# Kernel tuning notes

Measured on AMD Instinct MI355X. Metric: run time of the kernel, lower is better.

## Reference

```python
import jax, jax.numpy as jnp
import numpy as np

N, T = 32, 1500
ENC_DIM, DEC_DIM = 1024, 1024
ATT_DIM, ATT_HEAD = 512, 4
HA = ATT_DIM * ATT_HEAD


def setup_inputs() -> dict:
    key = jax.random.key(0)
    ks = jax.random.split(key, 12)
    enc_pad = jax.random.normal(ks[0], (N, T, ENC_DIM), dtype=jnp.float32)
    enc_len = jax.random.randint(ks[1], (N,), T // 2, T + 1)
    enc_len = enc_len.at[0].set(T)  # ensure max == T (original code assumes mask width == T)
    dec_prev = jax.random.normal(ks[2], (N, DEC_DIM), dtype=jnp.float32)
    ali_prev = jnp.zeros((N, T), dtype=jnp.float32)  # unused by forward
    s = 0.02
    W_enc = jax.random.normal(ks[3], (ENC_DIM, HA), dtype=jnp.float32) * s
    b_enc = jnp.zeros((HA,), dtype=jnp.float32)
    W_key = jax.random.normal(ks[4], (ENC_DIM, HA), dtype=jnp.float32) * s
    W_dec = jax.random.normal(ks[5], (DEC_DIM, HA), dtype=jnp.float32) * s
    W_ctx = jax.random.normal(ks[6], (HA, ENC_DIM), dtype=jnp.float32) * s
    b_ctx = jnp.zeros((ENC_DIM,), dtype=jnp.float32)
    # grouped Conv1d(HA -> H, kernel=1, groups=H, bias=False): weight [H, A]
    w_conv = jax.random.normal(ks[7], (ATT_HEAD, ATT_DIM), dtype=jnp.float32) * s
    return dict(enc_pad=enc_pad, enc_len=enc_len, dec_prev=dec_prev, ali_prev=ali_prev,
                W_enc=W_enc, b_enc=b_enc, W_key=W_key, W_dec=W_dec,
                W_ctx=W_ctx, b_ctx=b_ctx, w_conv=w_conv)


def reference(enc_pad, enc_len, dec_prev, ali_prev,
              W_enc, b_enc, W_key, W_dec, W_ctx, b_ctx, w_conv):
    n, t, _ = enc_pad.shape
    H, A = ATT_HEAD, ATT_DIM
    # enc_part: N x H x T x A
    enc_part = (enc_pad @ W_enc + b_enc).reshape(n, t, H, A).transpose(0, 2, 1, 3)
    # key_part: N x H x A x T
    key_part = (enc_pad @ W_key).reshape(n, t, H, A).transpose(0, 2, 3, 1)
    # dec_part: N x H x A
    dec_part = (dec_prev @ W_dec).reshape(n, H, A)
    # additive score: tanh(key + dec), grouped 1x1 conv scorer -> N x H x T
    sum_part = jnp.tanh(key_part + dec_part[:, :, :, None])
    e = jnp.einsum('nhat,ha->nht', sum_part, w_conv)
    # padding mask: True where t >= enc_len
    pad_mask = jnp.arange(t)[None, :] >= enc_len[:, None]  # N x T
    e = jnp.where(pad_mask[:, None, :], -jnp.inf, e)
    ali = jax.nn.softmax(e, axis=-1)  # N x H x T
    # weighted sum over time, then context projection
    ctx = jnp.einsum('nht,nhta->nha', ali, enc_part).reshape(n, H * A)
    ctx = ctx @ W_ctx + b_ctx  # N x D_enc
    return ali, ctx
```

## Files before the change

kernel.cpp:

```cpp
#include <hip/hip_runtime.h>
#include <hip/hip_bf16.h>


#define N_B   32
#define T_S   1500
#define ENC_D 1024
#define HA_D  2048
#define A_D   512
#define H_N   4
#define MROWS 48000

typedef short s8v  __attribute__((ext_vector_type(8)));
typedef float f32x4 __attribute__((ext_vector_type(4)));

__device__ __forceinline__ unsigned short f2bf(float f) {
    unsigned u = __float_as_uint(f);
    unsigned r = (u + 0x7FFFu + ((u >> 16) & 1u)) >> 16;
    return (unsigned short)r;
}
__device__ __forceinline__ float bf2f(unsigned short b) {
    return __uint_as_float(((unsigned)b) << 16);
}
__device__ __forceinline__ float fast_tanh(float x) {
    float e2 = __expf(2.0f * x);
    return 1.0f - __fdividef(2.0f, e2 + 1.0f);
}
__device__ __forceinline__ void gload_lds16(const void* g, void* l) {
    __builtin_amdgcn_global_load_lds(
        (const unsigned int __attribute__((address_space(1)))*)g,
        (unsigned int __attribute__((address_space(3)))*)l, 16, 0, 0);
}

__device__ __forceinline__ void skinny_body(
    int bid, const float* __restrict__ X, const float* __restrict__ W,
    const float* __restrict__ bias, float* __restrict__ Y,
    int Ncols, int ct_mask, int ct_shift, int xA, int xB, float* xT ) {
    const int tid = threadIdx.x;
    const int ct = bid & ct_mask, ks = bid >> ct_shift;
    const int c0 = ct << 8, k0 = ks << 6;
    const int hsel = c0 >> 9;
    {
        const int n = tid >> 3, kk0 = (tid & 7) << 3;
        const float* xr = X + (size_t)n * xA + hsel * xB + k0 + kk0;
        float4 v0 = *(const float4*)xr;
        float4 v1 = *(const float4*)(xr + 4);
        xT[(kk0 + 0) * 36 + n] = v0.x;
        xT[(kk0 + 1) * 36 + n] = v0.y;
        xT[(kk0 + 2) * 36 + n] = v0.z;
        xT[(kk0 + 3) * 36 + n] = v0.w;
        xT[(kk0 + 4) * 36 + n] = v1.x;
        xT[(kk0 + 5) * 36 + n] = v1.y;
        xT[(kk0 + 6) * 36 + n] = v1.z;
        xT[(kk0 + 7) * 36 + n] = v1.w;
    }
    __syncthreads();
    const int w = tid >> 6, lane = tid & 63;
    f32x4 acc[8];
    if (bias != nullptr && ks == 0) {
        f32x4 bv = *(const f32x4*)&bias[c0 + (lane << 2)];
#pragma unroll
        for (int j = 0; j < 8; ++j) acc[j] = bv;
    } else {
#pragma unroll
        for (int j = 0; j < 8; ++j) { f32x4 z = {0.f, 0.f, 0.f, 0.f}; acc[j] = z; }
    }
    const float* Wp = W + (size_t)k0 * Ncols + c0 + (lane << 2);
#pragma unroll 4
    for (int kk = 0; kk < 64; ++kk) {
        f32x4 wf = *(const f32x4*)(Wp + (size_t)kk * Ncols);
        f32x4 xlo = *(const f32x4*)&xT[kk * 36 + w * 8];
        f32x4 xhi = *(const f32x4*)&xT[kk * 36 + w * 8 + 4];
#pragma unroll
        for (int j = 0; j < 4; ++j) {
            acc[j]     += xlo[j] * wf;
            acc[4 + j] += xhi[j] * wf;
        }
    }
#pragma unroll
    for (int j = 0; j < 8; ++j) {
        float* yp = Y + (size_t)(w * 8 + j) * Ncols + c0 + (lane << 2);
#pragma unroll
        for (int i = 0; i < 4; ++i) atomicAdd(yp + i, acc[j][i]);
    }
}

__global__ __launch_bounds__(256) void skinny_k(
    const float* __restrict__ X, const float* __restrict__ W,
    const float* __restrict__ bias, float* __restrict__ Y,
    int Ncols, int ct_mask, int ct_shift, int xA, int xB) {
    __shared__ float xT[64 * 36];
    skinny_body(blockIdx.x, X, W, bias, Y, Ncols, ct_mask, ct_shift, xA, xB, xT);
}

__global__ __launch_bounds__(256) void prep_k(
    const float* __restrict__ enc_pad, const float* __restrict__ Wk,
    const float* __restrict__ dec_prev, const float* __restrict__ W_dec,
    unsigned short* __restrict__ Xb, unsigned short* __restrict__ Wt,
    float* __restrict__ dp) {
    __shared__ float shmem[64 * 65];
    const int b = blockIdx.x;
    const int tid = threadIdx.x;
    if (b < 128) {
        skinny_body(b, dec_prev, W_dec, nullptr, dp, HA_D, 7, 3, 1024, 0, shmem);
    } else if (b < 640) {
        float (*ld)[65] = (float(*)[65])shmem;
        const int bb = b - 128;
        const int tx = tid & 63, ty = tid >> 6;
        const int c0 = (bb & 31) * 64, d0 = (bb >> 5) * 64;
#pragma unroll
        for (int j = 0; j < 16; ++j)
            ld[ty + 4 * j][tx] = Wk[(size_t)(d0 + ty + 4 * j) * HA_D + c0 + tx];
        __syncthreads();
#pragma unroll
        for (int j = 0; j < 16; ++j)
            Wt[(size_t)(c0 + ty + 4 * j) * ENC_D + d0 + tx] = f2bf(ld[tx][ty + 4 * j]);
    } else {
        const float4* in = (const float4*)enc_pad;
        ushort4* out = (ushort4*)Xb;
        for (int i = (b - 640) * 256 + tid; i < 12288000; i += 3000 * 256) {
            float4 v = in[i];
            ushort4 o;
            o.x = f2bf(v.x); o.y = f2bf(v.y); o.z = f2bf(v.z); o.w = f2bf(v.w);
            out[i] = o;
        }
    }
}

__global__ __launch_bounds__(512) void fused_score_k(
    const unsigned short* __restrict__ Xb, const unsigned short* __restrict__ Wt,
    const float* __restrict__ dec, const float* __restrict__ wconv,
    const int* __restrict__ enc_len, float* __restrict__ e_out) {
    __shared__ unsigned short As[128 * 64];
    __shared__ unsigned short Bs[256 * 64];
    __shared__ float e_s[128];

    const int tid = threadIdx.x;
    const int lane = tid & 63, wid = tid >> 6;
    const int wr = wid >> 2, wc = wid & 3;
    const int l15 = lane & 15, lhi = lane >> 4;

    int orig = blockIdx.x;
    int wgid = (orig & 7) * 375 + (orig >> 3);
    const int mtile = wgid >> 3, nt = wgid & 7;
    const int r0 = mtile * 128;
    const int bcol0 = nt * 256;
    const int h = nt >> 1;

    {
        int n0 = (int)((unsigned)r0 / 1500u);
        int t0 = r0 - n0 * 1500;
        if (t0 + 127 < 1500 && t0 >= enc_len[n0]) return;
    }

    if (tid < 128) e_s[tid] = 0.f;

    const unsigned short* aSrc[2]; int aDst[2];
#pragma unroll
    for (int ld = 0; ld < 2; ++ld) {
        int li = ld * 512 + tid, rowL = li >> 3, c16 = li & 7;
        aSrc[ld] = Xb + (size_t)(r0 + rowL) * ENC_D + ((c16 ^ (rowL & 7)) << 3);
        aDst[ld] = li * 8;
    }
    const unsigned short* bSrc[4]; int bDst[4];
#pragma unroll
    for (int ld = 0; ld < 4; ++ld) {
        int li = ld * 512 + tid, colL = li >> 3, c16 = li & 7;
        bSrc[ld] = Wt + (size_t)(bcol0 + colL) * ENC_D + ((c16 ^ (colL & 7)) << 3);
        bDst[ld] = li * 8;
    }

    const int cA0 = (lhi * 8) ^ ((l15 & 7) << 3);
    const int cA1 = (32 + lhi * 8) ^ ((l15 & 7) << 3);
    const int arow = wr * 64 + l15;
    const int bcol = wc * 64 + l15;

    f32x4 acc[4][4];
#pragma unroll
    for (int m = 0; m < 4; ++m)
#pragma unroll
        for (int n2 = 0; n2 < 4; ++n2) {
            f32x4 z = {0.f, 0.f, 0.f, 0.f};
            acc[m][n2] = z;
        }

    for (int ks = 0; ks < 16; ++ks) {
        const int kb = ks << 6;
#pragma unroll
        for (int ld = 0; ld < 2; ++ld) gload_lds16(aSrc[ld] + kb, As + aDst[ld]);
#pragma unroll
        for (int ld = 0; ld < 4; ++ld) gload_lds16(bSrc[ld] + kb, Bs + bDst[ld]);
        __syncthreads();
#pragma unroll
        for (int kk = 0; kk < 2; ++kk) {
            const int cc = kk ? cA1 : cA0;
            s8v af[4], bv[4];
#pragma unroll
            for (int m = 0; m < 4; ++m)
                af[m] = *(const s8v*)&As[(arow + m * 16) * 64 + cc];
#pragma unroll
            for (int n2 = 0; n2 < 4; ++n2)
                bv[n2] = *(const s8v*)&Bs[(bcol + n2 * 16) * 64 + cc];
#pragma unroll
            for (int m = 0; m < 4; ++m)
#pragma unroll
                for (int n2 = 0; n2 < 4; ++n2)
                    acc[m][n2] = __builtin_amdgcn_mfma_f32_16x16x32_bf16(af[m], bv[n2], acc[m][n2], 0, 0, 0);
        }
        __syncthreads();
    }

    float wv[4];
#pragma unroll
    for (int n2 = 0; n2 < 4; ++n2)
        wv[n2] = wconv[bcol0 + wc * 64 + n2 * 16 + l15];
#pragma unroll
    for (int m = 0; m < 4; ++m) {
#pragma unroll
        for (int rg = 0; rg < 4; ++rg) {
            int row_l = wr * 64 + m * 16 + lhi * 4 + rg;
            int grow = r0 + row_l;
            int nn = (int)((unsigned)grow / 1500u);
            const float* dsl = dec + (size_t)nn * HA_D + bcol0 + wc * 64 + l15;
            float s = 0.f;
#pragma unroll
            for (int n2 = 0; n2 < 4; ++n2) {
                float v = acc[m][n2][rg] + dsl[n2 * 16];
                s += wv[n2] * fast_tanh(v);
            }
            s += __shfl_xor(s, 1); s += __shfl_xor(s, 2);
            s += __shfl_xor(s, 4); s += __shfl_xor(s, 8);
            if (l15 == 0) atomicAdd(&e_s[row_l], s);
        }
    }
    __syncthreads();
    if (tid < 128) {
        int grow = r0 + tid;
        int nn = grow / 1500, tt = grow - nn * 1500;
        atomicAdd(&e_out[(size_t)(nn * H_N + h) * T_S + tt], e_s[tid]);
    }
}

__global__ void softmax_k(const float* __restrict__ e, const int* __restrict__ enc_len,
                          float* __restrict__ ali, float* __restrict__ ctx_zero) {
    const int tid = threadIdx.x, lane = tid & 63, wid = tid >> 6;
    ctx_zero[blockIdx.x * 256 + tid] = 0.f;
    const int n = blockIdx.x >> 2;
    const int len = enc_len[n];
    const float* row = e + (size_t)blockIdx.x * T_S;
    float* orow = ali + (size_t)blockIdx.x * T_S;
    __shared__ float red[4];
    float p[6];
    float mx = -__builtin_inff();
#pragma unroll
    for (int i = 0; i < 6; ++i) {
        int t = tid + i * 256;
        float v = -__builtin_inff();
        if (t < T_S && t < len) v = row[t];
        p[i] = v;
        mx = fmaxf(mx, v);
    }
#pragma unroll
    for (int o = 32; o; o >>= 1) mx = fmaxf(mx, __shfl_xor(mx, o));
    if (lane == 0) red[wid] = mx;
    __syncthreads();
    mx = fmaxf(fmaxf(red[0], red[1]), fmaxf(red[2], red[3]));
    __syncthreads();
    float sum = 0.f;
#pragma unroll
    for (int i = 0; i < 6; ++i) {
        float qv = (p[i] == -__builtin_inff()) ? 0.f : __expf(p[i] - mx);
        p[i] = qv;
        sum += qv;
    }
#pragma unroll
    for (int o = 32; o; o >>= 1) sum += __shfl_xor(sum, o);
    if (lane == 0) red[wid] = sum;
    __syncthreads();
    sum = red[0] + red[1] + red[2] + red[3];
    float inv = 1.0f / sum;
#pragma unroll
    for (int i = 0; i < 6; ++i) {
        int t = tid + i * 256;
        if (t < T_S) orow[t] = p[i] * inv;
    }
}

__global__ __launch_bounds__(256) void wenc_k(const unsigned short* __restrict__ Xb,
                                              const float* __restrict__ ali,
                                              const int* __restrict__ enc_len,
                                              float* __restrict__ wenc) {
    const int tid = threadIdx.x;
    const int n = blockIdx.x & 31, tq = blockIdx.x >> 5;
    const int t0 = tq * 94;
    const int tcnt = (t0 + 94 <= T_S) ? 94 : (T_S - t0);
    if (t0 >= enc_len[n]) return;
    __shared__ float alis[4][94];
    for (int i = tid; i < 376; i += 256) {
        int hh = i / 94, tt = i - hh * 94;
        if (tt < tcnt) alis[hh][tt] = ali[(size_t)(n * H_N + hh) * T_S + t0 + tt];
    }
    __syncthreads();
    const int d0 = tid * 4;
    float a[4][4] = {};
    const unsigned short* xp = Xb + (size_t)(n * T_S + t0) * ENC_D + d0;
#pragma unroll 4
    for (int t = 0; t < tcnt; ++t) {
        ushort4 xv = *(const ushort4*)&xp[(size_t)t * ENC_D];
        float x0 = bf2f(xv.x), x1 = bf2f(xv.y), x2 = bf2f(xv.z), x3 = bf2f(xv.w);
#pragma unroll
        for (int hh = 0; hh < 4; ++hh) {
            float al = alis[hh][t];
            a[hh][0] = fmaf(al, x0, a[hh][0]);
            a[hh][1] = fmaf(al, x1, a[hh][1]);
            a[hh][2] = fmaf(al, x2, a[hh][2]);
            a[hh][3] = fmaf(al, x3, a[hh][3]);
        }
    }
#pragma unroll
    for (int hh = 0; hh < 4; ++hh)
#pragma unroll
        for (int j = 0; j < 4; ++j)
            atomicAdd(&wenc[(size_t)(n * H_N + hh) * ENC_D + d0 + j], a[hh][j]);
}

extern "C" void kernel_launch(void* const* d_in, const int* in_sizes, int n_in,
                              void* d_out, int out_size, void* d_ws, size_t ws_size,
                              hipStream_t stream) {
    const float* enc_pad  = (const float*)d_in[0];
    const int*   enc_len  = (const int*)d_in[1];
    const float* dec_prev = (const float*)d_in[2];
    const float* W_enc    = (const float*)d_in[4];
    const float* b_enc    = (const float*)d_in[5];
    const float* W_key    = (const float*)d_in[6];
    const float* W_dec    = (const float*)d_in[7];
    const float* W_ctx    = (const float*)d_in[8];
    const float* b_ctx    = (const float*)d_in[9];
    const float* w_conv   = (const float*)d_in[10];

    char* ws = (char*)d_ws;
    unsigned short* Xb = (unsigned short*)ws;
    unsigned short* Wt = (unsigned short*)(ws + 98304000);
    float* dp   = (float*)(ws + 102498304);
    float* e    = (float*)(ws + 102760448);
    float* wenc = (float*)(ws + 103528448);
    float* cpre = (float*)(ws + 104052736);

    float* ali = (float*)d_out;
    float* ctx = ((float*)d_out) + 192000;

    hipMemsetAsync(ws + 102498304, 0, 1816576, stream);
    prep_k<<<3640, 256, 0, stream>>>(enc_pad, W_key, dec_prev, W_dec, Xb, Wt, dp);
    fused_score_k<<<3000, 512, 0, stream>>>(Xb, Wt, dp, w_conv, enc_len, e);
    softmax_k<<<128, 256, 0, stream>>>(e, enc_len, ali, ctx);
    wenc_k<<<512, 256, 0, stream>>>(Xb, ali, enc_len, wenc);
    skinny_k<<<128, 256, 0, stream>>>(wenc, W_enc, b_enc, cpre, HA_D, 7, 3, 4096, 1024);
    skinny_k<<<128, 256, 0, stream>>>(cpre, W_ctx, b_ctx, ctx, ENC_D, 3, 2, 2048, 0);
}
```

Before: 405.5 us.

## Double-buffer score GEMM with 256-row tiles and restructure prep kernel

The fused score GEMM now uses 256x256 tiles with double-buffered LDS staging, interleaved fragment loads and MFMA issue, and raised wave priority during MFMA blocks. This is meant to hide global-to-LDS latency and raise per-load reuse. The prep kernel replaces the split-K atomic dec projection with 8 non-atomic blocks, folds the workspace memset into the kernel, and skips bf16 conversion of padded time rows past enc_len. The larger tile raises register and LDS pressure and needs clamping for the final partial tile.

```diff
diff --git a/kernel.cpp b/kernel.cpp
--- a/kernel.cpp
+++ b/kernel.cpp
@@ -30,6 +30,8 @@
         (const unsigned int __attribute__((address_space(1)))*)g,
         (unsigned int __attribute__((address_space(3)))*)l, 16, 0, 0);
 }
+
+#define BARRIER() do { asm volatile("" ::: "memory"); __builtin_amdgcn_s_barrier(); asm volatile("" ::: "memory"); } while (0)
 
 __device__ __forceinline__ void skinny_body(
     int bid, const float* __restrict__ X, const float* __restrict__ W,
@@ -95,16 +97,55 @@
 __global__ __launch_bounds__(256) void prep_k(
     const float* __restrict__ enc_pad, const float* __restrict__ Wk,
     const float* __restrict__ dec_prev, const float* __restrict__ W_dec,
+    const int* __restrict__ enc_len,
     unsigned short* __restrict__ Xb, unsigned short* __restrict__ Wt,
-    float* __restrict__ dp) {
+    float* __restrict__ dp, float* __restrict__ zbase) {
     __shared__ float shmem[64 * 65];
     const int b = blockIdx.x;
     const int tid = threadIdx.x;
-    if (b < 128) {
-        skinny_body(b, dec_prev, W_dec, nullptr, dp, HA_D, 7, 3, 1024, 0, shmem);
-    } else if (b < 640) {
+    if (b < 8) {
+        const int c0 = b << 8;
+        const int w = tid >> 6, lane = tid & 63;
+        f32x4 acc[8];
+#pragma unroll
+        for (int j = 0; j < 8; ++j) { f32x4 z = {0.f, 0.f, 0.f, 0.f}; acc[j] = z; }
+        for (int ks = 0; ks < 16; ++ks) {
+            const int k0 = ks << 6;
+            {
+                const int n = tid >> 3, kk0 = (tid & 7) << 3;
+                const float* xr = dec_prev + (size_t)n * 1024 + k0 + kk0;
+                float4 v0 = *(const float4*)xr;
+                float4 v1 = *(const float4*)(xr + 4);
+                shmem[(kk0 + 0) * 36 + n] = v0.x;
+                shmem[(kk0 + 1) * 36 + n] = v0.y;
+                shmem[(kk0 + 2) * 36 + n] = v0.z;
+                shmem[(kk0 + 3) * 36 + n] = v0.w;
+                shmem[(kk0 + 4) * 36 + n] = v1.x;
+                shmem[(kk0 + 5) * 36 + n] = v1.y;
+                shmem[(kk0 + 6) * 36 + n] = v1.z;
+                shmem[(kk0 + 7) * 36 + n] = v1.w;
+            }
+            __syncthreads();
+            const float* Wp = W_dec + (size_t)k0 * HA_D + c0 + (lane << 2);
+#pragma unroll 4
+            for (int kk = 0; kk < 64; ++kk) {
+                f32x4 wf = *(const f32x4*)(Wp + (size_t)kk * HA_D);
+                f32x4 xlo = *(const f32x4*)&shmem[kk * 36 + w * 8];
+                f32x4 xhi = *(const f32x4*)&shmem[kk * 36 + w * 8 + 4];
+#pragma unroll
+                for (int j = 0; j < 4; ++j) {
+                    acc[j]     += xlo[j] * wf;
+                    acc[4 + j] += xhi[j] * wf;
+                }
+            }
+            __syncthreads();
+        }
+#pragma unroll
+        for (int j = 0; j < 8; ++j)
+            *(f32x4*)&dp[(size_t)(w * 8 + j) * HA_D + c0 + (lane << 2)] = acc[j];
+    } else if (b < 520) {
         float (*ld)[65] = (float(*)[65])shmem;
-        const int bb = b - 128;
+        const int bb = b - 8;
         const int tx = tid & 63, ty = tid >> 6;
         const int c0 = (bb & 31) * 64, d0 = (bb >> 5) * 64;
 #pragma unroll
@@ -114,25 +155,56 @@
 #pragma unroll
         for (int j = 0; j < 16; ++j)
             Wt[(size_t)(c0 + ty + 4 * j) * ENC_D + d0 + tx] = f2bf(ld[tx][ty + 4 * j]);
+    } else if (b < 900) {
+        int zi = (b - 520) * 256 + tid;
+        if (zi < 97152) {
+            float4 z = {0.f, 0.f, 0.f, 0.f};
+            ((float4*)zbase)[zi] = z;
+        }
     } else {
-        const float4* in = (const float4*)enc_pad;
-        ushort4* out = (ushort4*)Xb;
-        for (int i = (b - 640) * 256 + tid; i < 12288000; i += 3000 * 256) {
-            float4 v = in[i];
-            ushort4 o;
-            o.x = f2bf(v.x); o.y = f2bf(v.y); o.z = f2bf(v.z); o.w = f2bf(v.w);
-            out[i] = o;
-        }
-    }
-}
-
-__global__ __launch_bounds__(512) void fused_score_k(
+        const int cb = b - 900;
+        const int n = cb / 94, tch = cb - n * 94;
+        const int t0 = tch * 16;
+        if (t0 >= enc_len[n]) return;
+        const int rmax = (1500 - t0 < 16) ? (1500 - t0) : 16;
+        const float4* in = (const float4*)enc_pad + ((size_t)n * 1500 + t0) * 256;
+        ushort4* out = (ushort4*)Xb + ((size_t)n * 1500 + t0) * 256;
+#pragma unroll
+        for (int it = 0; it < 16; ++it) {
+            int j = it * 256 + tid;
+            if ((j >> 8) < rmax) {
+                float4 v = in[j];
+                ushort4 o;
+                o.x = f2bf(v.x); o.y = f2bf(v.y); o.z = f2bf(v.z); o.w = f2bf(v.w);
+                out[j] = o;
+            }
+        }
+    }
+}
+
+
+#define LDQA(dst, MH, CC) { _Pragma("unroll") \
+    for (int i_ = 0; i_ < 4; ++i_) \
+        dst[i_] = *(const s8v*)&Ac[(arow + (MH) * 64 + i_ * 16) * 64 + (CC)]; }
+#define LDQB(dst, CC) { _Pragma("unroll") \
+    for (int n_ = 0; n_ < 4; ++n_) \
+        dst[n_] = *(const s8v*)&Bc[(bcol + n_ * 16) * 64 + (CC)]; }
+#define MFMAQ(MH, AF, BF) { __builtin_amdgcn_s_setprio(1); \
+    _Pragma("unroll") for (int i_ = 0; i_ < 4; ++i_) { \
+        _Pragma("unroll") for (int n_ = 0; n_ < 4; ++n_) \
+            acc[(MH) * 4 + i_][n_] = __builtin_amdgcn_mfma_f32_16x16x32_bf16((AF)[i_], (BF)[n_], acc[(MH) * 4 + i_][n_], 0, 0, 0); } \
+    __builtin_amdgcn_s_setprio(0); }
+#define STAGE(BUF, KB) { unsigned short* Ab_ = &As[BUF][0]; unsigned short* Bb_ = &Bs[BUF][0]; \
+    _Pragma("unroll") for (int q_ = 0; q_ < 4; ++q_) gload_lds16(aS[q_] + (KB), Ab_ + aD[q_]); \
+    _Pragma("unroll") for (int q_ = 0; q_ < 4; ++q_) gload_lds16(bS[q_] + (KB), Bb_ + bD[q_]); }
+
+__global__ __launch_bounds__(512, 2) void fused_score_k(
     const unsigned short* __restrict__ Xb, const unsigned short* __restrict__ Wt,
     const float* __restrict__ dec, const float* __restrict__ wconv,
     const int* __restrict__ enc_len, float* __restrict__ e_out) {
-    __shared__ unsigned short As[128 * 64];
-    __shared__ unsigned short Bs[256 * 64];
-    __shared__ float e_s[128];
+    __shared__ unsigned short As[2][16384];
+    __shared__ unsigned short Bs[2][16384];
+    __shared__ float e_s[256];
 
     const int tid = threadIdx.x;
     const int lane = tid & 63, wid = tid >> 6;
@@ -140,73 +212,75 @@
     const int l15 = lane & 15, lhi = lane >> 4;
 
     int orig = blockIdx.x;
-    int wgid = (orig & 7) * 375 + (orig >> 3);
+    int wgid = (orig & 7) * 188 + (orig >> 3);
     const int mtile = wgid >> 3, nt = wgid & 7;
-    const int r0 = mtile * 128;
+    const int r0 = mtile * 256;
     const int bcol0 = nt * 256;
     const int h = nt >> 1;
 
     {
         int n0 = (int)((unsigned)r0 / 1500u);
         int t0 = r0 - n0 * 1500;
-        if (t0 + 127 < 1500 && t0 >= enc_len[n0]) return;
-    }
-
-    if (tid < 128) e_s[tid] = 0.f;
-
-    const unsigned short* aSrc[2]; int aDst[2];
-#pragma unroll
-    for (int ld = 0; ld < 2; ++ld) {
-        int li = ld * 512 + tid, rowL = li >> 3, c16 = li & 7;
-        aSrc[ld] = Xb + (size_t)(r0 + rowL) * ENC_D + ((c16 ^ (rowL & 7)) << 3);
-        aDst[ld] = li * 8;
-    }
-    const unsigned short* bSrc[4]; int bDst[4];
-#pragma unroll
-    for (int ld = 0; ld < 4; ++ld) {
-        int li = ld * 512 + tid, colL = li >> 3, c16 = li & 7;
-        bSrc[ld] = Wt + (size_t)(bcol0 + colL) * ENC_D + ((c16 ^ (colL & 7)) << 3);
-        bDst[ld] = li * 8;
+        if (t0 + 255 < 1500 && t0 >= enc_len[n0]) return;
+    }
+
+    if (tid < 256) e_s[tid] = 0.f;
+
+    const unsigned short* aS[4]; int aD[4];
+    const unsigned short* bS[4]; int bD[4];
+#pragma unroll
+    for (int q = 0; q < 4; ++q) {
+        int hh = q >> 1, ld = q & 1;
+        int li = ld * 512 + tid, c16 = li & 7;
+        int rowL = hh * 128 + (li >> 3);
+        unsigned grow = (unsigned)(r0 + rowL);
+        if (grow > (unsigned)(MROWS - 1)) grow = MROWS - 1;
+        aS[q] = Xb + (size_t)grow * ENC_D + ((c16 ^ (rowL & 7)) << 3);
+        aD[q] = hh * 8192 + li * 8;
+        int colL = hh * 128 + (li >> 3);
+        bS[q] = Wt + (size_t)(bcol0 + colL) * ENC_D + ((c16 ^ (colL & 7)) << 3);
+        bD[q] = hh * 8192 + li * 8;
     }
 
     const int cA0 = (lhi * 8) ^ ((l15 & 7) << 3);
     const int cA1 = (32 + lhi * 8) ^ ((l15 & 7) << 3);
-    const int arow = wr * 64 + l15;
+    const int arow = wr * 128 + l15;
     const int bcol = wc * 64 + l15;
 
-    f32x4 acc[4][4];
-#pragma unroll
-    for (int m = 0; m < 4; ++m)
+    f32x4 acc[8][4];
+#pragma unroll
+    for (int m = 0; m < 8; ++m)
 #pragma unroll
         for (int n2 = 0; n2 < 4; ++n2) {
             f32x4 z = {0.f, 0.f, 0.f, 0.f};
             acc[m][n2] = z;
         }
 
-    for (int ks = 0; ks < 16; ++ks) {
-        const int kb = ks << 6;
-#pragma unroll
-        for (int ld = 0; ld < 2; ++ld) gload_lds16(aSrc[ld] + kb, As + aDst[ld]);
-#pragma unroll
-        for (int ld = 0; ld < 4; ++ld) gload_lds16(bSrc[ld] + kb, Bs + bDst[ld]);
-        __syncthreads();
-#pragma unroll
-        for (int kk = 0; kk < 2; ++kk) {
-            const int cc = kk ? cA1 : cA0;
-            s8v af[4], bv[4];
-#pragma unroll
-            for (int m = 0; m < 4; ++m)
-                af[m] = *(const s8v*)&As[(arow + m * 16) * 64 + cc];
-#pragma unroll
-            for (int n2 = 0; n2 < 4; ++n2)
-                bv[n2] = *(const s8v*)&Bs[(bcol + n2 * 16) * 64 + cc];
-#pragma unroll
-            for (int m = 0; m < 4; ++m)
-#pragma unroll
-                for (int n2 = 0; n2 < 4; ++n2)
-                    acc[m][n2] = __builtin_amdgcn_mfma_f32_16x16x32_bf16(af[m], bv[n2], acc[m][n2], 0, 0, 0);
-        }
-        __syncthreads();
+    STAGE(0, 0);
+    asm volatile("s_waitcnt vmcnt(0)" ::: "memory");
+    BARRIER();
+    int cur = 0;
+    const unsigned short* Ac = &As[0][0];
+    const unsigned short* Bc = &Bs[0][0];
+    s8v afA[4], afB[4], bfA[4], bfB[4];
+    LDQA(afA, 0, cA0); LDQB(bfA, cA0);
+
+    for (int kt = 0; kt < 16; ++kt) {
+        if (kt < 15) { STAGE(cur ^ 1, (kt + 1) << 6); }
+        LDQA(afB, 1, cA0);
+        MFMAQ(0, afA, bfA);
+        LDQA(afA, 0, cA1); LDQB(bfB, cA1);
+        MFMAQ(1, afB, bfA);
+        LDQA(afB, 1, cA1);
+        MFMAQ(0, afA, bfB);
+        MFMAQ(1, afB, bfB);
+        if (kt < 15) {
+            asm volatile("s_waitcnt vmcnt(0)" ::: "memory");
+            BARRIER();
+            cur ^= 1;
+            Ac = &As[cur][0]; Bc = &Bs[cur][0];
+            LDQA(afA, 0, cA0); LDQB(bfA, cA0);
+        }
     }
 
     float wv[4];
@@ -214,29 +288,33 @@
     for (int n2 = 0; n2 < 4; ++n2)
         wv[n2] = wconv[bcol0 + wc * 64 + n2 * 16 + l15];
 #pragma unroll
-    for (int m = 0; m < 4; ++m) {
+    for (int m = 0; m < 8; ++m) {
 #pragma unroll
         for (int rg = 0; rg < 4; ++rg) {
-            int row_l = wr * 64 + m * 16 + lhi * 4 + rg;
+            int row_l = wr * 128 + m * 16 + lhi * 4 + rg;
             int grow = r0 + row_l;
-            int nn = (int)((unsigned)grow / 1500u);
-            const float* dsl = dec + (size_t)nn * HA_D + bcol0 + wc * 64 + l15;
-            float s = 0.f;
-#pragma unroll
-            for (int n2 = 0; n2 < 4; ++n2) {
-                float v = acc[m][n2][rg] + dsl[n2 * 16];
-                s += wv[n2] * fast_tanh(v);
+            if (grow < MROWS) {
+                int nn = (int)((unsigned)grow / 1500u);
+                const float* dsl = dec + (size_t)nn * HA_D + bcol0 + wc * 64 + l15;
+                float s = 0.f;
+#pragma unroll
+                for (int n2 = 0; n2 < 4; ++n2) {
+                    float v = acc[m][n2][rg] + dsl[n2 * 16];
+                    s += wv[n2] * fast_tanh(v);
+                }
+                s += __shfl_xor(s, 1); s += __shfl_xor(s, 2);
+                s += __shfl_xor(s, 4); s += __shfl_xor(s, 8);
+                if (l15 == 0) atomicAdd(&e_s[row_l], s);
             }
-            s += __shfl_xor(s, 1); s += __shfl_xor(s, 2);
-            s += __shfl_xor(s, 4); s += __shfl_xor(s, 8);
-            if (l15 == 0) atomicAdd(&e_s[row_l], s);
-        }
-    }
-    __syncthreads();
-    if (tid < 128) {
+        }
+    }
+    __syncthreads();
+    if (tid < 256) {
         int grow = r0 + tid;
-        int nn = grow / 1500, tt = grow - nn * 1500;
-        atomicAdd(&e_out[(size_t)(nn * H_N + h) * T_S + tt], e_s[tid]);
+        if (grow < MROWS) {
+            int nn = grow / 1500, tt = grow - nn * 1500;
+            atomicAdd(&e_out[(size_t)(nn * H_N + h) * T_S + tt], e_s[tid]);
+        }
     }
 }
 
@@ -348,9 +426,8 @@
     float* ali = (float*)d_out;
     float* ctx = ((float*)d_out) + 192000;
 
-    hipMemsetAsync(ws + 102498304, 0, 1816576, stream);
-    prep_k<<<3640, 256, 0, stream>>>(enc_pad, W_key, dec_prev, W_dec, Xb, Wt, dp);
-    fused_score_k<<<3000, 512, 0, stream>>>(Xb, Wt, dp, w_conv, enc_len, e);
+    prep_k<<<3908, 256, 0, stream>>>(enc_pad, W_key, dec_prev, W_dec, enc_len, Xb, Wt, dp, e);
+    fused_score_k<<<1504, 512, 0, stream>>>(Xb, Wt, dp, w_conv, enc_len, e);
     softmax_k<<<128, 256, 0, stream>>>(e, enc_len, ali, ctx);
     wenc_k<<<512, 256, 0, stream>>>(Xb, ali, enc_len, wenc);
     skinny_k<<<128, 256, 0, stream>>>(wenc, W_enc, b_enc, cpre, HA_D, 7, 3, 4096, 1024);
```

Result: slower. 595.9 us (+47.0%).
